# Performance work log

Hardware: AMD Instinct MI355X
Metric: run time of the kernel (lower is better)

Reference implementation:

```python
import jax, jax.numpy as jnp
import numpy as np
import math

D, H, L, FF, V = 512, 8, 6, 2048, 512
DK = D // H
EPS = 1e-5


def _pos_encoding(seq_len, d_model):
    pos = np.arange(seq_len, dtype=np.float32)[:, None]
    div = np.exp(np.arange(0, d_model, 2, dtype=np.float32) * (-math.log(10000.0) / d_model))
    pe = np.zeros((seq_len, d_model), dtype=np.float32)
    pe[:, 0::2] = np.sin(pos * div)
    pe[:, 1::2] = np.cos(pos * div)
    return jnp.asarray(pe)


def _layernorm(x, g, b):
    mu = jnp.mean(x, axis=-1, keepdims=True)
    var = jnp.mean(jnp.square(x - mu), axis=-1, keepdims=True)
    return (x - mu) * jax.lax.rsqrt(var + EPS) * g + b


def setup_inputs() -> dict:
    key = jax.random.key(0)
    ks = jax.random.split(key, 16)
    B, S = 4, 1024
    inp = {
        'input_ids': jax.random.randint(ks[0], (B, S), 0, V, dtype=jnp.int64),
        'attention_mask': jnp.ones((B, S), dtype=jnp.int32),
        'emb': 0.02 * jax.random.normal(ks[1], (V, D), jnp.float32),
        # per-layer stacked params, torch Linear layout [out, in]
        'wq': 0.02 * jax.random.normal(ks[2], (L, D, D), jnp.float32),
        'bq': jnp.zeros((L, D), jnp.float32),
        'wk': 0.02 * jax.random.normal(ks[3], (L, D, D), jnp.float32),
        'bk': jnp.zeros((L, D), jnp.float32),
        'wv': 0.02 * jax.random.normal(ks[4], (L, D, D), jnp.float32),
        'bv': jnp.zeros((L, D), jnp.float32),
        'wo': 0.02 * jax.random.normal(ks[5], (L, D, D), jnp.float32),
        'bo': jnp.zeros((L, D), jnp.float32),
        'ln1_g': jnp.ones((L, D), jnp.float32),
        'ln1_b': jnp.zeros((L, D), jnp.float32),
        'w1': 0.02 * jax.random.normal(ks[6], (L, FF, D), jnp.float32),
        'b1': jnp.zeros((L, FF), jnp.float32),
        'w2': 0.02 * jax.random.normal(ks[7], (L, D, FF), jnp.float32),
        'b2': jnp.zeros((L, D), jnp.float32),
        'ln2_g': jnp.ones((L, D), jnp.float32),
        'ln2_b': jnp.zeros((L, D), jnp.float32),
        'lnf_g': jnp.ones((D,), jnp.float32),
        'lnf_b': jnp.zeros((D,), jnp.float32),
        'lm_w': 0.02 * jax.random.normal(ks[8], (V, D), jnp.float32),
    }
    return inp


def reference(input_ids, attention_mask, emb, wq, bq, wk, bk, wv, bv, wo, bo,
              ln1_g, ln1_b, w1, b1, w2, b2, ln2_g, ln2_b, lnf_g, lnf_b, lm_w):
    B, S = input_ids.shape
    x = emb[input_ids] * math.sqrt(D) + _pos_encoding(S, D)[None]  # [B,S,D]
    causal = jnp.tril(jnp.ones((S, S), jnp.float32))
    mask = causal[None, None] * attention_mask[:, None, None, :].astype(jnp.float32)  # [B,1,S,S]

    def step(h, p):
        (lwq, lbq, lwk, lbk, lwv, lbv, lwo, lbo, g1, be1, lw1, lb1, lw2, lb2, g2, be2) = p
        q = (jnp.einsum('bsd,ed->bse', h, lwq) + lbq).reshape(B, S, H, DK).transpose(0, 2, 1, 3)
        k = (jnp.einsum('bsd,ed->bse', h, lwk) + lbk).reshape(B, S, H, DK).transpose(0, 2, 1, 3)
        v = (jnp.einsum('bsd,ed->bse', h, lwv) + lbv).reshape(B, S, H, DK).transpose(0, 2, 1, 3)
        scores = jnp.einsum('bhqd,bhkd->bhqk', q, k) / math.sqrt(DK)
        scores = jnp.where(mask == 0, jnp.float32(-1e9), scores)
        attn = jax.nn.softmax(scores, axis=-1)
        o = jnp.einsum('bhqk,bhkd->bhqd', attn, v).transpose(0, 2, 1, 3).reshape(B, S, D)
        o = jnp.einsum('bsd,ed->bse', o, lwo) + lbo
        h = _layernorm(h + o, g1, be1)
        f = jax.nn.relu(jnp.einsum('bsd,fd->bsf', h, lw1) + lb1)
        f = jnp.einsum('bsf,df->bsd', f, lw2) + lb2
        h = _layernorm(h + f, g2, be2)
        return h, None

    x, _ = jax.lax.scan(step, x, (wq, bq, wk, bk, wv, bv, wo, bo,
                                  ln1_g, ln1_b, w1, b1, w2, b2, ln2_g, ln2_b))
    x = _layernorm(x, lnf_g, lnf_b)
    logits = jnp.einsum('bsd,vd->bsv', x, lm_w)  # [B,S,V]
    return logits
```

## Files before the change

### kernel.cpp

```cpp
#include <hip/hip_runtime.h>
#include <math.h>

#define D_MODEL 512
#define NHEAD   8
#define DKH     64
#define NLAYER  6
#define FFDIM   2048
#define VOCAB   512
#define BB      4
#define SS      1024
#define NROWS   4096

typedef unsigned short ushort_t;
typedef short short8 __attribute__((ext_vector_type(8)));
typedef float f32x4  __attribute__((ext_vector_type(4)));

__device__ __forceinline__ float bf2f(ushort_t u) {
    union { float f; unsigned int i; } x; x.i = ((unsigned int)u) << 16; return x.f;
}
__device__ __forceinline__ ushort_t f2bf(float f) {
    union { float f; unsigned int i; } x; x.f = f;
    unsigned int r = x.i + 0x7FFFu + ((x.i >> 16) & 1u);
    return (ushort_t)(r >> 16);
}
__device__ __forceinline__ void gload_lds16(const void* g, void* l) {
    __builtin_amdgcn_global_load_lds(
        (const __attribute__((address_space(1))) void*)g,
        (__attribute__((address_space(3))) void*)l, 16, 0, 0);
}

__global__ __launch_bounds__(256) void cvt_layer(
    const float* __restrict__ wq, const float* __restrict__ wk, const float* __restrict__ wv,
    const float* __restrict__ wo, const float* __restrict__ w1, const float* __restrict__ w2,
    const float* __restrict__ bq, const float* __restrict__ bk, const float* __restrict__ bv,
    ushort_t* __restrict__ wl, float* __restrict__ bqkv)
{
    int idx = blockIdx.x * 256 + threadIdx.x;
    int e = idx * 4;
    float4 v;
    if (e < 786432) {
        if (e < 262144)       v = *(const float4*)(wq + e);
        else if (e < 524288)  v = *(const float4*)(wk + (e - 262144));
        else                  v = *(const float4*)(wv + (e - 524288));
    } else if (e < 1048576)   v = *(const float4*)(wo + (e - 786432));
    else if (e < 2097152)     v = *(const float4*)(w1 + (e - 1048576));
    else                      v = *(const float4*)(w2 + (e - 2097152));
    union { ushort_t u[4]; uint2 q; } pk;
    pk.u[0] = f2bf(v.x); pk.u[1] = f2bf(v.y); pk.u[2] = f2bf(v.z); pk.u[3] = f2bf(v.w);
    *(uint2*)(wl + e) = pk.q;
    if (idx < 384) {
        int b4 = idx * 4;
        float4 bv4;
        if (b4 < 512)       bv4 = *(const float4*)(bq + b4);
        else if (b4 < 1024) bv4 = *(const float4*)(bk + (b4 - 512));
        else                bv4 = *(const float4*)(bv + (b4 - 1024));
        *(float4*)(bqkv + b4) = bv4;
    }
}

__global__ __launch_bounds__(256) void cvt_simple(
    const float* __restrict__ src, ushort_t* __restrict__ dst)
{
    int e = (blockIdx.x * 256 + threadIdx.x) * 4;
    float4 v = *(const float4*)(src + e);
    union { ushort_t u[4]; uint2 q; } pk;
    pk.u[0] = f2bf(v.x); pk.u[1] = f2bf(v.y); pk.u[2] = f2bf(v.z); pk.u[3] = f2bf(v.w);
    *(uint2*)(dst + e) = pk.q;
}

__global__ __launch_bounds__(256) void maskbias_kernel(
    const int* __restrict__ am, float* __restrict__ mb)
{
    int i = blockIdx.x * 256 + threadIdx.x;
    if (i < NROWS) mb[i] = am[i] ? 0.f : -1e9f;
}

__global__ __launch_bounds__(512) void embed_kernel(
    const int* __restrict__ ids, const float* __restrict__ emb,
    float* __restrict__ xf, ushort_t* __restrict__ xb)
{
    int row = blockIdx.x;
    int d   = threadIdx.x;
    int s   = row & (SS - 1);
    int tok = ids[row];
    float div = expf(-(float)(d & ~1) * 0.0179889460390586f);
    float arg = (float)s * div;
    float pe  = (d & 1) ? cosf(arg) : sinf(arg);
    float v = emb[(size_t)tok * D_MODEL + d] * 22.62741699796952f + pe;
    xf[(size_t)row * D_MODEL + d] = v;
    xb[(size_t)row * D_MODEL + d] = f2bf(v);
}

__global__ __launch_bounds__(512) void ln_kernel(
    const float* __restrict__ x, const float* __restrict__ g,
    const float* __restrict__ b, float* __restrict__ outf, ushort_t* __restrict__ outb)
{
    int row = blockIdx.x;
    int d   = threadIdx.x;
    int wave = d >> 6, lane = d & 63;
    __shared__ float red[8];

    float v = x[(size_t)row * D_MODEL + d];
    float s = v;
#pragma unroll
    for (int o = 32; o > 0; o >>= 1) s += __shfl_xor(s, o);
    if (lane == 0) red[wave] = s;
    __syncthreads();
    float tot = 0.f;
#pragma unroll
    for (int i = 0; i < 8; ++i) tot += red[i];
    float mu = tot * (1.0f / D_MODEL);
    float c  = v - mu;
    __syncthreads();
    float s2 = c * c;
#pragma unroll
    for (int o = 32; o > 0; o >>= 1) s2 += __shfl_xor(s2, o);
    if (lane == 0) red[wave] = s2;
    __syncthreads();
    float tot2 = 0.f;
#pragma unroll
    for (int i = 0; i < 8; ++i) tot2 += red[i];
    float var = tot2 * (1.0f / D_MODEL);
    float y = c * (1.0f / sqrtf(var + 1e-5f)) * g[d] + b[d];
    outf[(size_t)row * D_MODEL + d] = y;
    outb[(size_t)row * D_MODEL + d] = f2bf(y);
}

template<int BM, int BN, bool RELU, bool RES, bool OBF16, bool VT>
__global__ __launch_bounds__(256) void gemm_kernel(
    const ushort_t* __restrict__ A, const ushort_t* __restrict__ W,
    const float* __restrict__ bias, const float* __restrict__ res,
    void* __restrict__ out, ushort_t* __restrict__ vtg, int M, int N, int K)
{
    constexpr int WMT = BM / 2, WNT = BN / 2;
    constexpr int FM = WMT / 16, FN = WNT / 16;
    constexpr int ISSA = BM / 32, ISSB = BN / 32;
    __shared__ ushort_t As[BM * 64];
    __shared__ ushort_t Bs[BN * 64];

    const int t = threadIdx.x;
    const int w = t >> 6, lane = t & 63;
    const int wr = w >> 1, wc = w & 1;
    const int col0 = blockIdx.x * BN;
    const int row0 = blockIdx.y * BM;
    const int lrow = lane & 15, kg = lane >> 4;
    const int srow = t >> 3;
    const int sk8  = (t & 7) ^ ((t >> 3) & 7);

    f32x4 acc[FM][FN];
#pragma unroll
    for (int m = 0; m < FM; ++m)
#pragma unroll
        for (int n = 0; n < FN; ++n) acc[m][n] = (f32x4){0.f, 0.f, 0.f, 0.f};

    for (int k0 = 0; k0 < K; k0 += 64) {
#pragma unroll
        for (int i = 0; i < ISSA; ++i)
            gload_lds16(A + (size_t)(row0 + i * 32 + srow) * K + k0 + sk8 * 8,
                        (char*)As + i * 4096 + t * 16);
#pragma unroll
        for (int i = 0; i < ISSB; ++i)
            gload_lds16(W + (size_t)(col0 + i * 32 + srow) * K + k0 + sk8 * 8,
                        (char*)Bs + i * 4096 + t * 16);
        __syncthreads();
#pragma unroll
        for (int kk = 0; kk < 2; ++kk) {
            short8 af[FM], bfv[FN];
#pragma unroll
            for (int m = 0; m < FM; ++m) {
                const int row = wr * WMT + m * 16 + lrow;
                af[m] = *(const short8*)&As[row * 64 + (((kk * 4 + kg) ^ (lrow & 7)) << 3)];
            }
#pragma unroll
            for (int n = 0; n < FN; ++n) {
                const int col = wc * WNT + n * 16 + lrow;
                bfv[n] = *(const short8*)&Bs[col * 64 + (((kk * 4 + kg) ^ (lrow & 7)) << 3)];
            }
#pragma unroll
            for (int m = 0; m < FM; ++m)
#pragma unroll
                for (int n = 0; n < FN; ++n)
                    acc[m][n] = __builtin_amdgcn_mfma_f32_16x16x32_bf16(
                        af[m], bfv[n], acc[m][n], 0, 0, 0);
        }
        __syncthreads();
    }

    const int lrow4 = (lane >> 4) * 4;
    const int lcol  = lane & 15;
#pragma unroll
    for (int m = 0; m < FM; ++m)
#pragma unroll
        for (int n = 0; n < FN; ++n) {
            const int col = col0 + wc * WNT + n * 16 + lcol;
            const float bv = bias ? bias[col] : 0.f;
            const int row_base = row0 + wr * WMT + m * 16 + lrow4;
            if (VT && col >= 1024) {
                const int vh = (col - 1024) >> 6;
                const int vd = (col - 1024) & 63;
                const int bq = row_base >> 10;
                const int s0 = row_base & 1023;
                union { ushort_t u[4]; uint2 q; } pk;
#pragma unroll
                for (int j = 0; j < 4; ++j) pk.u[j] = f2bf(acc[m][n][j] + bv);
                *(uint2*)(vtg + ((size_t)(bq * 8 + vh) * 64 + vd) * 1024 + s0) = pk.q;
            } else {
#pragma unroll
                for (int j = 0; j < 4; ++j) {
                    const int row = row_base + j;
                    float v = acc[m][n][j] + bv;
                    if (RES)  v += res[(size_t)row * N + col];
                    if (RELU) v = fmaxf(v, 0.f);
                    if (OBF16) ((ushort_t*)out)[(size_t)row * N + col] = f2bf(v);
                    else       ((float*)out)[(size_t)row * N + col] = v;
                }
            }
        }
}

__global__ __launch_bounds__(256) void attn_kernel(
    const ushort_t* __restrict__ qkv, const ushort_t* __restrict__ vtg,
    const float* __restrict__ mbias, ushort_t* __restrict__ o)
{
    __shared__ ushort_t Kl[2][64 * 64];
    __shared__ ushort_t Vl[2][64 * 64];

    const int t = threadIdx.x, w = t >> 6, l = t & 63;
    const int bid = blockIdx.x;
    const int qt = 15 - (bid >> 5);
    const int bh = bid & 31, b = bh >> 3, h = bh & 7;
    const int q0 = qt * 64;
    const int lg = l >> 4, lr = l & 15;
    const int qi = q0 + w * 16 + lr;

    const ushort_t* qrow = qkv + (size_t)(b * SS + qi) * 1536 + h * 64;
    const short8 qa0 = *(const short8*)(qrow + lg * 8);
    const short8 qa1 = *(const short8*)(qrow + 32 + lg * 8);

    float m_run = -1e30f, l_run = 0.f;
    f32x4 oacc[4];
#pragma unroll
    for (int nb = 0; nb < 4; ++nb) oacc[nb] = (f32x4){0.f, 0.f, 0.f, 0.f};

    const int krow = 32 * ((lr >> 1) & 1) + 8 * (lr >> 2) + (lr & 1);
    const ushort_t* qkvK = qkv + (size_t)(b * SS) * 1536 + 512 + h * 64;
    const ushort_t* vtgB = vtg + (size_t)bh * 64 * 1024;
    const float*    mb0  = mbias + b * SS + 8 * lg;

    const int sr0 = t >> 3, sc0 = t & 7;

    auto STAGE = [&](int buf, int kt) {
#pragma unroll
        for (int p = 0; p < 2; ++p) {
            const int row = p * 32 + sr0;
            const int ch  = sc0 ^ ((row >> 3) & 7);
            gload_lds16(qkvK + (size_t)(kt * 64 + row) * 1536 + ch * 8,
                        (char*)&Kl[buf][0] + (p * 256 + t) * 16);
        }
#pragma unroll
        for (int p = 0; p < 2; ++p) {
            const int row = p * 32 + sr0;
            const int ch  = sc0 ^ (row & 7);
            gload_lds16(vtgB + (size_t)row * 1024 + kt * 64 + ch * 8,
                        (char*)&Vl[buf][0] + (p * 256 + t) * 16);
        }
    };

    auto COMPUTE = [&](int buf, int kt) {
        const ushort_t* Kb = &Kl[buf][0];
        const ushort_t* Vb = &Vl[buf][0];
        short8 kf[8], vf[8];
#pragma unroll
        for (int nf = 0; nf < 4; ++nf) {
            const int row = 2 * nf + krow;
            const int sw  = (row >> 3) & 7;
            kf[2 * nf]     = *(const short8*)&Kb[row * 64 + ((lg ^ sw) << 3)];
            kf[2 * nf + 1] = *(const short8*)&Kb[row * 64 + (((4 + lg) ^ sw) << 3)];
        }
#pragma unroll
        for (int nb = 0; nb < 4; ++nb) {
            const int row = 16 * nb + lr;
            const int sw  = row & 7;
            vf[2 * nb]     = *(const short8*)&Vb[row * 64 + ((lg ^ sw) << 3)];
            vf[2 * nb + 1] = *(const short8*)&Vb[row * 64 + (((4 + lg) ^ sw) << 3)];
        }
        const float* mrow = mb0 + kt * 64;
        const float4 mA = *(const float4*)(mrow);
        const float4 mB = *(const float4*)(mrow + 4);
        const float4 mC = *(const float4*)(mrow + 32);
        const float4 mD = *(const float4*)(mrow + 36);
        f32x4 s[4];
#pragma unroll
        for (int nf = 0; nf < 4; ++nf) {
            f32x4 a = (f32x4){0.f, 0.f, 0.f, 0.f};
            a = __builtin_amdgcn_mfma_f32_16x16x32_bf16(kf[2 * nf],     qa0, a, 0, 0, 0);
            a = __builtin_amdgcn_mfma_f32_16x16x32_bf16(kf[2 * nf + 1], qa1, a, 0, 0, 0);
            s[nf] = a;
        }
        const bool diag = (kt == qt);
        const int kbase = kt * 64 + 8 * lg;
#pragma unroll
        for (int nf = 0; nf < 4; ++nf) {
#pragma unroll
            for (int r = 0; r < 4; ++r) {
                const int e = r & 1, oo = (r >> 1) & 1;
                const int idx = 2 * nf + e;
                const float bias = oo ? (idx < 4 ? ((const float*)&mC)[idx] : ((const float*)&mD)[idx - 4])
                                      : (idx < 4 ? ((const float*)&mA)[idx] : ((const float*)&mB)[idx - 4]);
                float sv = s[nf][r] * 0.125f + bias;
                if (diag && (kbase + idx + 32 * oo) > qi) sv = -1e9f;
                s[nf][r] = sv;
            }
        }
        float pm[4];
#pragma unroll
        for (int nf = 0; nf < 4; ++nf)
            pm[nf] = fmaxf(fmaxf(s[nf][0], s[nf][1]), fmaxf(s[nf][2], s[nf][3]));
        float mx = fmaxf(fmaxf(pm[0], pm[1]), fmaxf(pm[2], pm[3]));
        mx = fmaxf(mx, __shfl_xor(mx, 16));
        mx = fmaxf(mx, __shfl_xor(mx, 32));
        const float mnew = fmaxf(m_run, mx);
        const float rs   = __expf(m_run - mnew);
        m_run = mnew;
        float ps[4];
#pragma unroll
        for (int nf = 0; nf < 4; ++nf) {
#pragma unroll
            for (int r = 0; r < 4; ++r) s[nf][r] = __expf(s[nf][r] - mnew);
            ps[nf] = (s[nf][0] + s[nf][1]) + (s[nf][2] + s[nf][3]);
        }
        float tsum = (ps[0] + ps[1]) + (ps[2] + ps[3]);
        tsum += __shfl_xor(tsum, 16);
        tsum += __shfl_xor(tsum, 32);
        l_run = l_run * rs + tsum;
#pragma unroll
        for (int nb = 0; nb < 4; ++nb)
#pragma unroll
            for (int r = 0; r < 4; ++r) oacc[nb][r] *= rs;
        union { unsigned u[4]; short8 s8; } pa0u, pa1u;
#pragma unroll
        for (int nf = 0; nf < 4; ++nf) {
            pa0u.u[nf] = ((unsigned)f2bf(s[nf][1]) << 16) | (unsigned)f2bf(s[nf][0]);
            pa1u.u[nf] = ((unsigned)f2bf(s[nf][3]) << 16) | (unsigned)f2bf(s[nf][2]);
        }
#pragma unroll
        for (int nb = 0; nb < 4; ++nb) {
            oacc[nb] = __builtin_amdgcn_mfma_f32_16x16x32_bf16(vf[2 * nb],     pa0u.s8, oacc[nb], 0, 0, 0);
            oacc[nb] = __builtin_amdgcn_mfma_f32_16x16x32_bf16(vf[2 * nb + 1], pa1u.s8, oacc[nb], 0, 0, 0);
        }
    };

    STAGE(0, 0);
    asm volatile("s_waitcnt vmcnt(0)" ::: "memory");
    __syncthreads();
    int buf = 0;
    for (int kt = 0; kt <= qt; ++kt) {
        if (kt < qt) STAGE(buf ^ 1, kt + 1);
        COMPUTE(buf, kt);
        asm volatile("s_waitcnt vmcnt(0)" ::: "memory");
        __syncthreads();
        buf ^= 1;
    }

    const float inv = 1.0f / l_run;
    ushort_t* orow = o + (size_t)(b * SS + qi) * 512 + h * 64;
#pragma unroll
    for (int nb = 0; nb < 4; ++nb) {
        union { ushort_t u[4]; uint2 q; } pk;
#pragma unroll
        for (int r = 0; r < 4; ++r) pk.u[r] = f2bf(oacc[nb][r] * inv);
        *(uint2*)(orow + nb * 16 + 4 * lg) = pk.q;
    }
}

extern "C" void kernel_launch(void* const* d_in, const int* in_sizes, int n_in,
                              void* d_out, int out_size, void* d_ws, size_t ws_size,
                              hipStream_t stream)
{
    const int*   ids   = (const int*)d_in[0];
    const int*   am    = (const int*)d_in[1];
    const float* emb   = (const float*)d_in[2];
    const float* wq    = (const float*)d_in[3];
    const float* bq    = (const float*)d_in[4];
    const float* wk    = (const float*)d_in[5];
    const float* bk    = (const float*)d_in[6];
    const float* wv    = (const float*)d_in[7];
    const float* bv    = (const float*)d_in[8];
    const float* wo    = (const float*)d_in[9];
    const float* bo    = (const float*)d_in[10];
    const float* ln1g  = (const float*)d_in[11];
    const float* ln1b  = (const float*)d_in[12];
    const float* w1    = (const float*)d_in[13];
    const float* b1    = (const float*)d_in[14];
    const float* w2    = (const float*)d_in[15];
    const float* b2    = (const float*)d_in[16];
    const float* ln2g  = (const float*)d_in[17];
    const float* ln2b  = (const float*)d_in[18];
    const float* lnfg  = (const float*)d_in[19];
    const float* lnfb  = (const float*)d_in[20];
    const float* lmw   = (const float*)d_in[21];

    char* base = (char*)d_ws;
    float*    h    = (float*)(base);
    float*    h2   = (float*)(base + 8388608);
    ushort_t* hb   = (ushort_t*)(base + 16777216);
    ushort_t* act  = (ushort_t*)(base + 20971520);
    ushort_t* qkvb = act;
    ushort_t* ob   = act + 6291456;
    ushort_t* fbuf = act;
    ushort_t* wl   = (ushort_t*)(base + 37748736);
    float*    bqkv = (float*)(base + 44040192);
    ushort_t* lmwb = (ushort_t*)(base + 44046336);
    float*    mbias= (float*)(base + 44570624);
    ushort_t* vtg  = (ushort_t*)h2;

    cvt_simple<<<256, 256, 0, stream>>>(lmw, lmwb);
    maskbias_kernel<<<16, 256, 0, stream>>>(am, mbias);
    embed_kernel<<<NROWS, 512, 0, stream>>>(ids, emb, h, hb);

    for (int l = 0; l < NLAYER; ++l) {
        const size_t dd = (size_t)l * 262144;
        const size_t fd = (size_t)l * 1048576;
        cvt_layer<<<3072, 256, 0, stream>>>(wq + dd, wk + dd, wv + dd, wo + dd,
                                            w1 + fd, w2 + fd,
                                            bq + l * 512, bk + l * 512, bv + l * 512,
                                            wl, bqkv);
        gemm_kernel<64, 128, false, false, true, true><<<dim3(12, 64), 256, 0, stream>>>(
            hb, wl, bqkv, nullptr, qkvb, vtg, NROWS, 1536, 512);

        attn_kernel<<<512, 256, 0, stream>>>(qkvb, vtg, mbias, ob);

        gemm_kernel<64, 64, false, true, false, false><<<dim3(8, 64), 256, 0, stream>>>(
            ob, wl + 786432, bo + l * 512, h, h2, nullptr, NROWS, 512, 512);
        ln_kernel<<<NROWS, 512, 0, stream>>>(h2, ln1g + l * 512, ln1b + l * 512, h, hb);

        gemm_kernel<64, 128, true, false, true, false><<<dim3(16, 64), 256, 0, stream>>>(
            hb, wl + 1048576, b1 + l * 2048, nullptr, fbuf, nullptr, NROWS, 2048, 512);
        gemm_kernel<64, 64, false, true, false, false><<<dim3(8, 64), 256, 0, stream>>>(
            fbuf, wl + 2097152, b2 + l * 512, h, h2, nullptr, NROWS, 512, 2048);
        ln_kernel<<<NROWS, 512, 0, stream>>>(h2, ln2g + l * 512, ln2b + l * 512, h, hb);
    }

    ln_kernel<<<NROWS, 512, 0, stream>>>(h, lnfg, lnfb, h, hb);
    gemm_kernel<64, 64, false, false, false, false><<<dim3(8, 64), 256, 0, stream>>>(
        hb, lmwb, nullptr, nullptr, d_out, nullptr, NROWS, 512, 512);
}
```

Before: 723.3 us.

## Convert all layer weights in one launch, remap GEMM blocks per XCD, raise MFMA priority

When the workspace is large enough, all six layers' weights are converted to bf16 by a single kernel up front, replacing six per-layer conversion launches. The GEMM kernel now remaps block IDs so that consecutive tiles land on the same XCD chunk, aiming for better L2 locality. The attention kernel raises wave priority around its MFMA sections. The one-pass path depends on the workspace size check and uses more workspace memory.

```diff
diff --git a/kernel.cpp b/kernel.cpp
--- a/kernel.cpp
+++ b/kernel.cpp
@@ -58,6 +58,39 @@
     }
 }
 
+__global__ __launch_bounds__(256) void cvt_all(
+    const float* __restrict__ wq, const float* __restrict__ wk, const float* __restrict__ wv,
+    const float* __restrict__ wo, const float* __restrict__ w1, const float* __restrict__ w2,
+    const float* __restrict__ bq, const float* __restrict__ bk, const float* __restrict__ bv,
+    ushort_t* __restrict__ wl, float* __restrict__ bqkv)
+{
+    int idx = blockIdx.x * 256 + threadIdx.x;
+    int e = idx * 4;
+    int l = e / 3145728;
+    int off = e - l * 3145728;
+    float4 v;
+    if (off < 786432) {
+        if (off < 262144)       v = *(const float4*)(wq + l * 262144 + off);
+        else if (off < 524288)  v = *(const float4*)(wk + l * 262144 + (off - 262144));
+        else                    v = *(const float4*)(wv + l * 262144 + (off - 524288));
+    } else if (off < 1048576)   v = *(const float4*)(wo + l * 262144 + (off - 786432));
+    else if (off < 2097152)     v = *(const float4*)(w1 + l * 1048576 + (off - 1048576));
+    else                        v = *(const float4*)(w2 + l * 1048576 + (off - 2097152));
+    union { ushort_t u[4]; uint2 q; } pk;
+    pk.u[0] = f2bf(v.x); pk.u[1] = f2bf(v.y); pk.u[2] = f2bf(v.z); pk.u[3] = f2bf(v.w);
+    *(uint2*)(wl + e) = pk.q;
+    if (idx < 2304) {
+        int b4 = idx * 4;
+        int bl = b4 / 1536;
+        int r  = b4 - bl * 1536;
+        float4 bv4;
+        if (r < 512)       bv4 = *(const float4*)(bq + bl * 512 + r);
+        else if (r < 1024) bv4 = *(const float4*)(bk + bl * 512 + (r - 512));
+        else               bv4 = *(const float4*)(bv + bl * 512 + (r - 1024));
+        *(float4*)(bqkv + b4) = bv4;
+    }
+}
+
 __global__ __launch_bounds__(256) void cvt_simple(
     const float* __restrict__ src, ushort_t* __restrict__ dst)
 {
@@ -141,8 +174,14 @@
     const int t = threadIdx.x;
     const int w = t >> 6, lane = t & 63;
     const int wr = w >> 1, wc = w & 1;
-    const int col0 = blockIdx.x * BN;
-    const int row0 = blockIdx.y * BM;
+
+    const int nwg  = gridDim.x * gridDim.y;
+    const int bidl = blockIdx.y * gridDim.x + blockIdx.x;
+    const int chunk = nwg >> 3;
+    const int wg = (bidl & 7) * chunk + (bidl >> 3);
+    const int col0 = (wg % gridDim.x) * BN;
+    const int row0 = (wg / gridDim.x) * BM;
+
     const int lrow = lane & 15, kg = lane >> 4;
     const int srow = t >> 3;
     const int sk8  = (t & 7) ^ ((t >> 3) & 7);
@@ -290,6 +329,7 @@
         const float4 mC = *(const float4*)(mrow + 32);
         const float4 mD = *(const float4*)(mrow + 36);
         f32x4 s[4];
+        __builtin_amdgcn_s_setprio(1);
 #pragma unroll
         for (int nf = 0; nf < 4; ++nf) {
             f32x4 a = (f32x4){0.f, 0.f, 0.f, 0.f};
@@ -297,6 +337,7 @@
             a = __builtin_amdgcn_mfma_f32_16x16x32_bf16(kf[2 * nf + 1], qa1, a, 0, 0, 0);
             s[nf] = a;
         }
+        __builtin_amdgcn_s_setprio(0);
         const bool diag = (kt == qt);
         const int kbase = kt * 64 + 8 * lg;
 #pragma unroll
@@ -343,11 +384,13 @@
             pa0u.u[nf] = ((unsigned)f2bf(s[nf][1]) << 16) | (unsigned)f2bf(s[nf][0]);
             pa1u.u[nf] = ((unsigned)f2bf(s[nf][3]) << 16) | (unsigned)f2bf(s[nf][2]);
         }
+        __builtin_amdgcn_s_setprio(1);
 #pragma unroll
         for (int nb = 0; nb < 4; ++nb) {
             oacc[nb] = __builtin_amdgcn_mfma_f32_16x16x32_bf16(vf[2 * nb],     pa0u.s8, oacc[nb], 0, 0, 0);
             oacc[nb] = __builtin_amdgcn_mfma_f32_16x16x32_bf16(vf[2 * nb + 1], pa1u.s8, oacc[nb], 0, 0, 0);
         }
+        __builtin_amdgcn_s_setprio(0);
     };
 
     STAGE(0, 0);
@@ -408,36 +451,55 @@
     ushort_t* qkvb = act;
     ushort_t* ob   = act + 6291456;
     ushort_t* fbuf = act;
+    ushort_t* vtg  = (ushort_t*)h2;
+
+    const bool onep = ws_size >= (size_t)76100000;
     ushort_t* wl   = (ushort_t*)(base + 37748736);
-    float*    bqkv = (float*)(base + 44040192);
-    ushort_t* lmwb = (ushort_t*)(base + 44046336);
-    float*    mbias= (float*)(base + 44570624);
-    ushort_t* vtg  = (ushort_t*)h2;
+    float*    bqkv; ushort_t* lmwb; float* mbias;
+    if (onep) {
+        bqkv  = (float*)(base + 75497472);
+        lmwb  = (ushort_t*)(base + 75534336);
+        mbias = (float*)(base + 76058624);
+    } else {
+        bqkv  = (float*)(base + 44040192);
+        lmwb  = (ushort_t*)(base + 44046336);
+        mbias = (float*)(base + 44570624);
+    }
 
     cvt_simple<<<256, 256, 0, stream>>>(lmw, lmwb);
     maskbias_kernel<<<16, 256, 0, stream>>>(am, mbias);
     embed_kernel<<<NROWS, 512, 0, stream>>>(ids, emb, h, hb);
+    if (onep)
+        cvt_all<<<18432, 256, 0, stream>>>(wq, wk, wv, wo, w1, w2, bq, bk, bv, wl, bqkv);
 
     for (int l = 0; l < NLAYER; ++l) {
         const size_t dd = (size_t)l * 262144;
         const size_t fd = (size_t)l * 1048576;
-        cvt_layer<<<3072, 256, 0, stream>>>(wq + dd, wk + dd, wv + dd, wo + dd,
-                                            w1 + fd, w2 + fd,
-                                            bq + l * 512, bk + l * 512, bv + l * 512,
-                                            wl, bqkv);
+        ushort_t* lw; const float* lb;
+        if (onep) {
+            lw = wl + (size_t)l * 3145728;
+            lb = bqkv + l * 1536;
+        } else {
+            cvt_layer<<<3072, 256, 0, stream>>>(wq + dd, wk + dd, wv + dd, wo + dd,
+                                                w1 + fd, w2 + fd,
+                                                bq + l * 512, bk + l * 512, bv + l * 512,
+                                                wl, bqkv);
+            lw = wl;
+            lb = bqkv;
+        }
         gemm_kernel<64, 128, false, false, true, true><<<dim3(12, 64), 256, 0, stream>>>(
-            hb, wl, bqkv, nullptr, qkvb, vtg, NROWS, 1536, 512);
+            hb, lw, lb, nullptr, qkvb, vtg, NROWS, 1536, 512);
 
         attn_kernel<<<512, 256, 0, stream>>>(qkvb, vtg, mbias, ob);
 
         gemm_kernel<64, 64, false, true, false, false><<<dim3(8, 64), 256, 0, stream>>>(
-            ob, wl + 786432, bo + l * 512, h, h2, nullptr, NROWS, 512, 512);
+            ob, lw + 786432, bo + l * 512, h, h2, nullptr, NROWS, 512, 512);
         ln_kernel<<<NROWS, 512, 0, stream>>>(h2, ln1g + l * 512, ln1b + l * 512, h, hb);
 
         gemm_kernel<64, 128, true, false, true, false><<<dim3(16, 64), 256, 0, stream>>>(
-            hb, wl + 1048576, b1 + l * 2048, nullptr, fbuf, nullptr, NROWS, 2048, 512);
+            hb, lw + 1048576, b1 + l * 2048, nullptr, fbuf, nullptr, NROWS, 2048, 512);
         gemm_kernel<64, 64, false, true, false, false><<<dim3(8, 64), 256, 0, stream>>>(
-            fbuf, wl + 2097152, b2 + l * 512, h, h2, nullptr, NROWS, 512, 2048);
+            fbuf, lw + 2097152, b2 + l * 512, h, h2, nullptr, NROWS, 512, 2048);
         ln_kernel<<<NROWS, 512, 0, stream>>>(h2, ln2g + l * 512, ln2b + l * 512, h, hb);
     }
 
```

Result: slower. 739.1 us (+2.2%).
